# Performance work log

Measured on AMD Instinct MI355X. Metric: run time of the kernel, lower is better.

The kernel has to match this reference:

```python
import jax, jax.numpy as jnp
import numpy as np

N_NODES = 100000
N_EDGES = 3200000
C = 50           # out_channels (== in_channels here, so no zero-padding needed)
L = 3            # num_layers
EDGE_TYPES = 2


def setup_inputs() -> dict:
    key = jax.random.key(0)
    ks = jax.random.split(key, 12)
    s = 1.0 / np.sqrt(C)
    x = jax.random.normal(ks[0], (N_NODES, C), dtype=jnp.float32)
    edge_index = jax.random.randint(ks[1], (2, N_EDGES), 0, N_NODES)
    edge_attr = jax.random.randint(ks[2], (N_EDGES,), 0, EDGE_TYPES)
    conv_weight = jax.random.uniform(ks[3], (L, C, C), jnp.float32, -s, s)
    w_ih = jax.random.uniform(ks[4], (3 * C, C), jnp.float32, -s, s)
    w_hh = jax.random.uniform(ks[5], (3 * C, C), jnp.float32, -s, s)
    b_ih = jax.random.uniform(ks[6], (3 * C,), jnp.float32, -s, s)
    b_hh = jax.random.uniform(ks[7], (3 * C,), jnp.float32, -s, s)
    edge_emb = jax.random.normal(ks[8], (EDGE_TYPES, C), dtype=jnp.float32)
    lin_w = jax.random.uniform(ks[9], (C, C), jnp.float32, -s, s)
    lin_b = jax.random.uniform(ks[10], (C,), jnp.float32, -s, s)
    return dict(x=x, edge_index=edge_index, edge_attr=edge_attr,
                conv_weight=conv_weight, w_ih=w_ih, w_hh=w_hh,
                b_ih=b_ih, b_hh=b_hh, edge_emb=edge_emb,
                lin_w=lin_w, lin_b=lin_b)


def _gru_cell(m, h, w_ih, w_hh, b_ih, b_hh):
    # torch.nn.GRUCell math
    gi = m @ w_ih.T + b_ih            # [N, 3C]
    gh = h @ w_hh.T + b_hh            # [N, 3C]
    i_r, i_z, i_n = jnp.split(gi, 3, axis=-1)
    h_r, h_z, h_n = jnp.split(gh, 3, axis=-1)
    r = jax.nn.sigmoid(i_r + h_r)
    z = jax.nn.sigmoid(i_z + h_z)
    n = jnp.tanh(i_n + r * h_n)
    return (1.0 - z) * n + z * h


def reference(x, edge_index, edge_attr, conv_weight, w_ih, w_hh,
              b_ih, b_hh, edge_emb, lin_w, lin_b):
    # edge embeddings are computed but unused in the original forward
    _ = edge_emb[edge_attr]
    src, dst = edge_index[0], edge_index[1]  # flow: source -> target
    h = x  # in_channels == out_channels, so no padding
    for i in range(L):
        m = h @ conv_weight[i]                               # [N, C]
        msg = jnp.take(m, src, axis=0)                       # gather  [E, C]
        agg = jax.ops.segment_sum(msg, dst, num_segments=N_NODES)  # scatter-add
        h = _gru_cell(agg, h, w_ih, w_hh, b_ih, b_hh)
    out = jax.nn.relu(h) @ lin_w.T + lin_b
    return out
```

## Files before the change

### kernel.cpp

```cpp
#include <hip/hip_runtime.h>
#include <hip/hip_fp16.h>

#define N_NODES 100000
#define N_EDGES 3200000
#define C 50
#define PH 64
#define NH (N_NODES * PH)
#define NTILES (N_NODES / 16)
#define NB2 391
#define BSH2 8
#define BMSK2 255
#define BCAP2 9216
#define EPB 4096
#define EB  ((N_EDGES + EPB - 1) / EPB)
#define EPT (EPB / 256)

typedef _Float16 half8 __attribute__((ext_vector_type(8)));
typedef float floatx4 __attribute__((ext_vector_type(4)));


__global__ __launch_bounds__(256) void partition_kernel(const int* __restrict__ ei,
                                                        int* __restrict__ cnt,
                                                        unsigned int* __restrict__ pairs) {
    __shared__ int hist[NB2];
    __shared__ int base[NB2];
    int e0 = blockIdx.x * EPB;
    int b[EPT]; unsigned int p[EPT];
#pragma unroll
    for (int i = 0; i < EPT; ++i) {
        int e = e0 + i * 256 + threadIdx.x;
        bool ok = e < N_EDGES;
        int d = ok ? ei[N_EDGES + e] : 0;
        int s = ok ? ei[e] : 0;
        b[i] = ok ? (d >> BSH2) : -1;
        p[i] = ((unsigned)s << BSH2) | (unsigned)(d & BMSK2);
    }
    for (int t = threadIdx.x; t < NB2; t += 256) hist[t] = 0;
    __syncthreads();
#pragma unroll
    for (int i = 0; i < EPT; ++i)
        if (b[i] >= 0) atomicAdd(&hist[b[i]], 1);
    __syncthreads();
    for (int t = threadIdx.x; t < NB2; t += 256)
        base[t] = hist[t] ? (t * BCAP2 + atomicAdd(&cnt[t], hist[t])) : 0;
    __syncthreads();
    for (int t = threadIdx.x; t < NB2; t += 256) hist[t] = 0;
    __syncthreads();
#pragma unroll
    for (int i = 0; i < EPT; ++i) {
        if (b[i] >= 0) {
            int r = atomicAdd(&hist[b[i]], 1);
            pairs[base[b[i]] + r] = p[i];
        }
    }
}

__global__ __launch_bounds__(1024) void bscan_kernel(const int* __restrict__ cnt,
                                                     int* __restrict__ bucketOff) {
    __shared__ int buf[1024];
    int t = threadIdx.x;
    int v = (t < NB2) ? cnt[t] : 0;
    buf[t] = v;
    __syncthreads();
    for (int off = 1; off < 1024; off <<= 1) {
        int tv = (t >= off) ? buf[t - off] : 0;
        __syncthreads();
        buf[t] += tv;
        __syncthreads();
    }
    if (t < NB2) {
        int excl = buf[t] - v;
        bucketOff[t] = excl;
        if (t == NB2 - 1) bucketOff[NB2] = excl + v;
    }
}

__global__ __launch_bounds__(256) void bucket_fill_kernel(const unsigned int* __restrict__ pairs,
                                                          const int* __restrict__ cnt,
                                                          const int* __restrict__ bucketOff,
                                                          int* __restrict__ rowptr,
                                                          int* __restrict__ col) {
    __shared__ int deg[256];
    __shared__ int cur[256];
    int b = blockIdx.x;
    int nbase = b << BSH2;
    int n_e = cnt[b];
    int slot0 = b * BCAP2;
    int segB = bucketOff[b];
    int tid = threadIdx.x;
    deg[tid] = 0;
    __syncthreads();
    for (int e = tid; e < n_e; e += 256)
        atomicAdd(&deg[pairs[slot0 + e] & BMSK2], 1);
    __syncthreads();
    int v = deg[tid];
    cur[tid] = v;
    __syncthreads();
    for (int off = 1; off < 256; off <<= 1) {
        int t = (tid >= off) ? cur[tid - off] : 0;
        __syncthreads();
        cur[tid] += t;
        __syncthreads();
    }
    int excl = cur[tid] - v;
    int n = nbase + tid;
    if (n < N_NODES) rowptr[n] = segB + excl;
    __syncthreads();
    cur[tid] = excl;
    __syncthreads();
    for (int e = tid; e < n_e; e += 256) {
        unsigned int p = pairs[slot0 + e];
        int r = atomicAdd(&cur[p & BMSK2], 1);
        col[segB + r] = (int)(p >> BSH2);
    }
    if (b == 0 && tid == 0) rowptr[N_NODES] = N_EDGES;
}

__global__ __launch_bounds__(256) void init_kernel(const float* __restrict__ x,
                                                   const float* __restrict__ conv_w,
                                                   const float* __restrict__ w_ih,
                                                   const float* __restrict__ w_hh,
                                                   const float* __restrict__ lin_w,
                                                   _Float16* __restrict__ h0,
                                                   _Float16* __restrict__ wb,
                                                   int* __restrict__ cnt) {
    int t = blockIdx.x * 256 + threadIdx.x;
    if (t < NH) {
        int n = t >> 6, c = t & 63;
        h0[t] = (c < C) ? (_Float16)x[n * C + c] : (_Float16)0.f;
    }
    if (t < 10 * 4096) {
        int mat = t >> 12, idx = t & 4095, n = idx >> 6, k = idx & 63;
        float v = 0.f;
        if (n < C && k < C) {
            if (mat < 3)      v = conv_w[mat * C * C + k * C + n];
            else if (mat < 6) v = w_ih[((mat - 3) * C + n) * C + k];
            else if (mat < 9) v = w_hh[((mat - 6) * C + n) * C + k];
            else              v = lin_w[n * C + k];
        }
        wb[t] = (_Float16)v;
    }
    if (t < NB2) cnt[t] = 0;
}

__device__ inline half8 load_a16(const _Float16* __restrict__ base, int row, int ks, int lane) {
    return *(const half8*)(base + (size_t)row * PH + (ks << 5) + ((lane >> 4) << 3));
}

__device__ inline half8 load_b_frag(const _Float16* __restrict__ wb, int nt, int ks, int lane) {
    const _Float16* p = wb + (((nt << 4) + (lane & 15)) << 6) + (ks << 5) + ((lane >> 4) << 3);
    return *(const half8*)p;
}

__device__ inline half8 load_b_lds(const _Float16* swb, int mat, int nt, int ks, int lane) {
    return *(const half8*)(swb + mat * 4608 + ((nt << 4) + (lane & 15)) * 72 + (ks << 5) + ((lane >> 4) << 3));
}

__device__ inline float sigmoidf_(float x) { return 1.f / (1.f + __expf(-x)); }
__device__ inline float tanhf_(float x)    { return 2.f * sigmoidf_(2.f * x) - 1.f; }

__global__ __launch_bounds__(256) void gemm_conv(const _Float16* __restrict__ h,
                                                 const _Float16* __restrict__ wb,
                                                 _Float16* __restrict__ m_h) {
    int wid = threadIdx.x >> 6, lane = threadIdx.x & 63;
    int tile = blockIdx.x * 4 + wid;
    if (tile >= NTILES) return;
    int base = tile * 16;
    int arow = base + (lane & 15);
    half8 a0 = load_a16(h, arow, 0, lane);
    half8 a1 = load_a16(h, arow, 1, lane);
#pragma unroll
    for (int nt = 0; nt < 4; ++nt) {
        floatx4 acc = {0.f, 0.f, 0.f, 0.f};
        acc = __builtin_amdgcn_mfma_f32_16x16x32_f16(a0, load_b_frag(wb, nt, 0, lane), acc, 0, 0, 0);
        acc = __builtin_amdgcn_mfma_f32_16x16x32_f16(a1, load_b_frag(wb, nt, 1, lane), acc, 0, 0, 0);
        int col = (nt << 4) + (lane & 15);
#pragma unroll
        for (int e = 0; e < 4; ++e) {
            int row = base + ((lane >> 4) << 2) + e;
            m_h[(size_t)row * PH + col] = (_Float16)acc[e];
        }
    }
}

__global__ __launch_bounds__(256) void gemm_gru_conv(const _Float16* __restrict__ agg,
                                                     const _Float16* __restrict__ hin,
                                                     const _Float16* __restrict__ wb_ih,
                                                     const _Float16* __restrict__ wb_hh,
                                                     const float* __restrict__ b_ih,
                                                     const float* __restrict__ b_hh,
                                                     const _Float16* __restrict__ wb_conv,
                                                     _Float16* __restrict__ hout,
                                                     _Float16* __restrict__ m_h) {
    __shared__ __align__(16) _Float16 swb[6 * 4608];
    __shared__ __align__(16) _Float16 hlds[4][16][72];
    int wid = threadIdx.x >> 6, lane = threadIdx.x & 63;
    int tile = blockIdx.x * 4 + wid;
    bool act = tile < NTILES;
    int base = tile * 16;
    int lrow = lane & 15, lgrp = lane >> 4;
    for (int i = threadIdx.x; i < 3072; i += 256) {
        int g = i << 3;
        int m = g >> 12, rem = g & 4095, row = rem >> 6, colc = rem & 63;
        *(half8*)&swb[m * 4608 + row * 72 + colc] = *(const half8*)(wb_ih + g);
    }
    half8 aA[2], aH[2];
    if (act) {
        int arow = base + lrow;
#pragma unroll
        for (int ks = 0; ks < 2; ++ks) {
            aA[ks] = load_a16(agg, arow, ks, lane);
            aH[ks] = load_a16(hin, arow, ks, lane);
        }
        *(half8*)&hlds[wid][lrow][lgrp << 3]        = aH[0];
        *(half8*)&hlds[wid][lrow][32 + (lgrp << 3)] = aH[1];
    }
    __syncthreads();
    if (act) {
#pragma unroll
        for (int nt = 0; nt < 4; ++nt) {
            int colc = (nt << 4) + lrow;
            bool cok = colc < C;
            float r_[4], z_[4];
            {
                floatx4 aI = {0.f,0.f,0.f,0.f}, aHc = {0.f,0.f,0.f,0.f};
#pragma unroll
                for (int ks = 0; ks < 2; ++ks) {
                    aI  = __builtin_amdgcn_mfma_f32_16x16x32_f16(aA[ks], load_b_lds(swb, 0, nt, ks, lane), aI, 0, 0, 0);
                    aHc = __builtin_amdgcn_mfma_f32_16x16x32_f16(aH[ks], load_b_lds(swb, 3, nt, ks, lane), aHc, 0, 0, 0);
                }
                float bi = cok ? b_ih[colc] : 0.f;
                float bh = cok ? b_hh[colc] : 0.f;
#pragma unroll
                for (int e = 0; e < 4; ++e) r_[e] = sigmoidf_((aI[e] + bi) + (aHc[e] + bh));
            }
            {
                floatx4 aI = {0.f,0.f,0.f,0.f}, aHc = {0.f,0.f,0.f,0.f};
#pragma unroll
                for (int ks = 0; ks < 2; ++ks) {
                    aI  = __builtin_amdgcn_mfma_f32_16x16x32_f16(aA[ks], load_b_lds(swb, 1, nt, ks, lane), aI, 0, 0, 0);
                    aHc = __builtin_amdgcn_mfma_f32_16x16x32_f16(aH[ks], load_b_lds(swb, 4, nt, ks, lane), aHc, 0, 0, 0);
                }
                float bi = cok ? b_ih[C + colc] : 0.f;
                float bh = cok ? b_hh[C + colc] : 0.f;
#pragma unroll
                for (int e = 0; e < 4; ++e) z_[e] = sigmoidf_((aI[e] + bi) + (aHc[e] + bh));
            }
            {
                floatx4 aI = {0.f,0.f,0.f,0.f}, aHc = {0.f,0.f,0.f,0.f};
#pragma unroll
                for (int ks = 0; ks < 2; ++ks) {
                    aI  = __builtin_amdgcn_mfma_f32_16x16x32_f16(aA[ks], load_b_lds(swb, 2, nt, ks, lane), aI, 0, 0, 0);
                    aHc = __builtin_amdgcn_mfma_f32_16x16x32_f16(aH[ks], load_b_lds(swb, 5, nt, ks, lane), aHc, 0, 0, 0);
                }
                float bi = cok ? b_ih[2 * C + colc] : 0.f;
                float bh = cok ? b_hh[2 * C + colc] : 0.f;
#pragma unroll
                for (int e = 0; e < 4; ++e) {
                    int rl = (lgrp << 2) + e;
                    int row = base + rl;
                    _Float16 val = (_Float16)0.f;
                    if (cok) {
                        float hv = (float)hlds[wid][rl][colc];
                        float nn = tanhf_((aI[e] + bi) + r_[e] * (aHc[e] + bh));
                        float z = z_[e];
                        val = (_Float16)((1.f - z) * nn + z * hv);
                    }
                    hout[(size_t)row * PH + colc] = val;
                    hlds[wid][rl][colc] = val;
                }
            }
        }
    }
    __syncthreads();
    if (act) {
        half8 a0 = *(const half8*)&hlds[wid][lrow][lgrp << 3];
        half8 a1 = *(const half8*)&hlds[wid][lrow][32 + (lgrp << 3)];
#pragma unroll
        for (int nt = 0; nt < 4; ++nt) {
            floatx4 acc = {0.f, 0.f, 0.f, 0.f};
            acc = __builtin_amdgcn_mfma_f32_16x16x32_f16(a0, load_b_frag(wb_conv, nt, 0, lane), acc, 0, 0, 0);
            acc = __builtin_amdgcn_mfma_f32_16x16x32_f16(a1, load_b_frag(wb_conv, nt, 1, lane), acc, 0, 0, 0);
            int col = (nt << 4) + lrow;
#pragma unroll
            for (int e = 0; e < 4; ++e) {
                int row = base + (lgrp << 2) + e;
                m_h[(size_t)row * PH + col] = (_Float16)acc[e];
            }
        }
    }
}

__global__ __launch_bounds__(256) void gemm_gru_out(const _Float16* __restrict__ agg,
                                                    const _Float16* __restrict__ hin,
                                                    const _Float16* __restrict__ wb_ih,
                                                    const _Float16* __restrict__ wb_hh,
                                                    const float* __restrict__ b_ih,
                                                    const float* __restrict__ b_hh,
                                                    const _Float16* __restrict__ wb_out,
                                                    const float* __restrict__ lin_b,
                                                    float* __restrict__ out) {
    __shared__ __align__(16) _Float16 swb[6 * 4608];
    __shared__ __align__(16) _Float16 hlds[4][16][72];
    int wid = threadIdx.x >> 6, lane = threadIdx.x & 63;
    int tile = blockIdx.x * 4 + wid;
    bool act = tile < NTILES;
    int base = tile * 16;
    int lrow = lane & 15, lgrp = lane >> 4;
    for (int i = threadIdx.x; i < 3072; i += 256) {
        int g = i << 3;
        int m = g >> 12, rem = g & 4095, row = rem >> 6, colc = rem & 63;
        *(half8*)&swb[m * 4608 + row * 72 + colc] = *(const half8*)(wb_ih + g);
    }
    half8 aA[2], aH[2];
    if (act) {
        int arow = base + lrow;
#pragma unroll
        for (int ks = 0; ks < 2; ++ks) {
            aA[ks] = load_a16(agg, arow, ks, lane);
            aH[ks] = load_a16(hin, arow, ks, lane);
        }
        *(half8*)&hlds[wid][lrow][lgrp << 3]        = aH[0];
        *(half8*)&hlds[wid][lrow][32 + (lgrp << 3)] = aH[1];
    }
    __syncthreads();
    if (act) {
#pragma unroll
        for (int nt = 0; nt < 4; ++nt) {
            int colc = (nt << 4) + lrow;
            bool cok = colc < C;
            float r_[4], z_[4];
            {
                floatx4 aI = {0.f,0.f,0.f,0.f}, aHc = {0.f,0.f,0.f,0.f};
#pragma unroll
                for (int ks = 0; ks < 2; ++ks) {
                    aI  = __builtin_amdgcn_mfma_f32_16x16x32_f16(aA[ks], load_b_lds(swb, 0, nt, ks, lane), aI, 0, 0, 0);
                    aHc = __builtin_amdgcn_mfma_f32_16x16x32_f16(aH[ks], load_b_lds(swb, 3, nt, ks, lane), aHc, 0, 0, 0);
                }
                float bi = cok ? b_ih[colc] : 0.f;
                float bh = cok ? b_hh[colc] : 0.f;
#pragma unroll
                for (int e = 0; e < 4; ++e) r_[e] = sigmoidf_((aI[e] + bi) + (aHc[e] + bh));
            }
            {
                floatx4 aI = {0.f,0.f,0.f,0.f}, aHc = {0.f,0.f,0.f,0.f};
#pragma unroll
                for (int ks = 0; ks < 2; ++ks) {
                    aI  = __builtin_amdgcn_mfma_f32_16x16x32_f16(aA[ks], load_b_lds(swb, 1, nt, ks, lane), aI, 0, 0, 0);
                    aHc = __builtin_amdgcn_mfma_f32_16x16x32_f16(aH[ks], load_b_lds(swb, 4, nt, ks, lane), aHc, 0, 0, 0);
                }
                float bi = cok ? b_ih[C + colc] : 0.f;
                float bh = cok ? b_hh[C + colc] : 0.f;
#pragma unroll
                for (int e = 0; e < 4; ++e) z_[e] = sigmoidf_((aI[e] + bi) + (aHc[e] + bh));
            }
            {
                floatx4 aI = {0.f,0.f,0.f,0.f}, aHc = {0.f,0.f,0.f,0.f};
#pragma unroll
                for (int ks = 0; ks < 2; ++ks) {
                    aI  = __builtin_amdgcn_mfma_f32_16x16x32_f16(aA[ks], load_b_lds(swb, 2, nt, ks, lane), aI, 0, 0, 0);
                    aHc = __builtin_amdgcn_mfma_f32_16x16x32_f16(aH[ks], load_b_lds(swb, 5, nt, ks, lane), aHc, 0, 0, 0);
                }
                float bi = cok ? b_ih[2 * C + colc] : 0.f;
                float bh = cok ? b_hh[2 * C + colc] : 0.f;
#pragma unroll
                for (int e = 0; e < 4; ++e) {
                    int rl = (lgrp << 2) + e;
                    _Float16 val = (_Float16)0.f;
                    if (cok) {
                        float hv = (float)hlds[wid][rl][colc];
                        float nn = tanhf_((aI[e] + bi) + r_[e] * (aHc[e] + bh));
                        float z = z_[e];
                        float h3 = (1.f - z) * nn + z * hv;
                        val = (_Float16)(h3 > 0.f ? h3 : 0.f);
                    }
                    hlds[wid][rl][colc] = val;
                }
            }
        }
    }
    __syncthreads();
    if (act) {
        half8 a0 = *(const half8*)&hlds[wid][lrow][lgrp << 3];
        half8 a1 = *(const half8*)&hlds[wid][lrow][32 + (lgrp << 3)];
#pragma unroll
        for (int nt = 0; nt < 4; ++nt) {
            floatx4 acc = {0.f, 0.f, 0.f, 0.f};
            acc = __builtin_amdgcn_mfma_f32_16x16x32_f16(a0, load_b_frag(wb_out, nt, 0, lane), acc, 0, 0, 0);
            acc = __builtin_amdgcn_mfma_f32_16x16x32_f16(a1, load_b_frag(wb_out, nt, 1, lane), acc, 0, 0, 0);
            int col = (nt << 4) + lrow;
            if (col < C) {
                float b = lin_b[col];
#pragma unroll
                for (int e = 0; e < 4; ++e) {
                    int row = base + (lgrp << 2) + e;
                    out[(size_t)row * C + col] = acc[e] + b;
                }
            }
        }
    }
}

__global__ __launch_bounds__(256) void gather_kernel(const __half* __restrict__ m_h,
                                                     const int* __restrict__ rowptr,
                                                     const int* __restrict__ col,
                                                     _Float16* __restrict__ agg) {
    int w = (blockIdx.x * 256 + threadIdx.x) >> 6;
    int lane = threadIdx.x & 63;
    if (w >= N_NODES) return;
    int start = rowptr[w], end = rowptr[w + 1];
    int j = lane >> 3, q = lane & 7;
    bool qok = (q < 7);
    int hoff = qok ? (q * 8) : 48;
    float acc0 = 0.f, acc1 = 0.f, acc2 = 0.f, acc3 = 0.f;
    float acc4 = 0.f, acc5 = 0.f, acc6 = 0.f, acc7 = 0.f;

    for (int base = start; base < end; base += 64) {
        int cidx = base + lane;
        int cols = col[cidx < N_EDGES ? cidx : (N_EDGES - 1)];
        int cnt = end - base; if (cnt > 64) cnt = 64;
        int nt8 = (cnt + 7) >> 3;
#pragma unroll 4
        for (int t = 0; t < nt8; ++t) {
            int rel = 8 * t + j;
            int s = __shfl(cols, rel);
            bool valid = qok && (rel < cnt);
            const uint4 v = *reinterpret_cast<const uint4*>(m_h + (size_t)s * PH + hoff);
            float2 f0 = __half22float2(*reinterpret_cast<const __half2*>(&v.x));
            float2 f1 = __half22float2(*reinterpret_cast<const __half2*>(&v.y));
            float2 f2 = __half22float2(*reinterpret_cast<const __half2*>(&v.z));
            float2 f3 = __half22float2(*reinterpret_cast<const __half2*>(&v.w));
            acc0 += valid ? f0.x : 0.f;  acc1 += valid ? f0.y : 0.f;
            acc2 += valid ? f1.x : 0.f;  acc3 += valid ? f1.y : 0.f;
            acc4 += valid ? f2.x : 0.f;  acc5 += valid ? f2.y : 0.f;
            acc6 += valid ? f3.x : 0.f;  acc7 += valid ? f3.y : 0.f;
        }
    }
#pragma unroll
    for (int s = 8; s <= 32; s <<= 1) {
        acc0 += __shfl_xor(acc0, s); acc1 += __shfl_xor(acc1, s);
        acc2 += __shfl_xor(acc2, s); acc3 += __shfl_xor(acc3, s);
        acc4 += __shfl_xor(acc4, s); acc5 += __shfl_xor(acc5, s);
        acc6 += __shfl_xor(acc6, s); acc7 += __shfl_xor(acc7, s);
    }
    if (j == 0) {
        if (qok) {
            half8 o;
            o[0] = (_Float16)acc0; o[1] = (_Float16)acc1;
            o[2] = (_Float16)acc2; o[3] = (_Float16)acc3;
            o[4] = (_Float16)acc4; o[5] = (_Float16)acc5;
            o[6] = (_Float16)acc6; o[7] = (_Float16)acc7;
            *reinterpret_cast<half8*>(agg + (size_t)w * PH + q * 8) = o;
        } else {
            half8 z = {};
            *reinterpret_cast<half8*>(agg + (size_t)w * PH + 56) = z;
        }
    }
}

extern "C" void kernel_launch(void* const* d_in, const int* in_sizes, int n_in,
                              void* d_out, int out_size, void* d_ws, size_t ws_size,
                              hipStream_t stream) {
    const float* x      = (const float*)d_in[0];
    const int*   ei     = (const int*)  d_in[1];
    const float* conv_w = (const float*)d_in[3];
    const float* w_ih   = (const float*)d_in[4];
    const float* w_hh   = (const float*)d_in[5];
    const float* b_ih   = (const float*)d_in[6];
    const float* b_hh   = (const float*)d_in[7];
    const float* lin_w  = (const float*)d_in[9];
    const float* lin_b  = (const float*)d_in[10];
    float* out = (float*)d_out;

    _Float16* h0  = (_Float16*)d_ws;
    _Float16* h1  = h0 + NH;
    _Float16* agg = h1 + NH;
    _Float16* m_h = agg + NH;
    _Float16* wb  = m_h + NH;
    unsigned int* pairs = (unsigned int*)agg;
    int* col       = (int*)(wb + 10 * 4096);
    int* rowptr    = col + N_EDGES;
    int* cnt       = rowptr + N_NODES + 1;
    int* bucketOff = cnt + NB2;

    const int initBlocks = (NH + 255) / 256;
    const int waveBlocks = (N_NODES * 64 + 255) / 256;
    const int gemmBlocks = (NTILES + 3) / 4;

    init_kernel<<<initBlocks, 256, 0, stream>>>(x, conv_w, w_ih, w_hh, lin_w, h0, wb, cnt);

    partition_kernel<<<EB, 256, 0, stream>>>(ei, cnt, pairs);
    bscan_kernel<<<1, 1024, 0, stream>>>(cnt, bucketOff);
    bucket_fill_kernel<<<NB2, 256, 0, stream>>>(pairs, cnt, bucketOff, rowptr, col);

    gemm_conv<<<gemmBlocks, 256, 0, stream>>>(h0, wb + 0 * 4096, m_h);
    gather_kernel<<<waveBlocks, 256, 0, stream>>>((const __half*)m_h, rowptr, col, agg);
    gemm_gru_conv<<<gemmBlocks, 256, 0, stream>>>(agg, h0, wb + 3 * 4096, wb + 6 * 4096,
                                                  b_ih, b_hh, wb + 1 * 4096, h1, m_h);
    gather_kernel<<<waveBlocks, 256, 0, stream>>>((const __half*)m_h, rowptr, col, agg);
    gemm_gru_conv<<<gemmBlocks, 256, 0, stream>>>(agg, h1, wb + 3 * 4096, wb + 6 * 4096,
                                                  b_ih, b_hh, wb + 2 * 4096, h0, m_h);
    gather_kernel<<<waveBlocks, 256, 0, stream>>>((const __half*)m_h, rowptr, col, agg);
    gemm_gru_out<<<gemmBlocks, 256, 0, stream>>>(agg, h0, wb + 3 * 4096, wb + 6 * 4096,
                                                 b_ih, b_hh, wb + 9 * 4096, lin_b, out);
}
```

Measured before the change: 377.5 us.

## Fold conv weights into GRU input weights and gather raw hidden state

Because aggregation is linear, (A·h)·W_conv·W_ih^T equals A·h·(W_conv·W_ih^T). The per-layer product of conv weight and GRU input weight is now precomputed in init, so each layer gathers h directly and the separate conv GEMM and m_h write are gone. The GRU kernels stage combined ih and hh weights from separate buffers. It also halves edges per block in partitioning. The folded product is rounded to fp16, which slightly changes numerics, and init does more FMA work per weight element.

```diff
diff --git a/kernel.cpp b/kernel.cpp
--- a/kernel.cpp
+++ b/kernel.cpp
@@ -11,7 +11,7 @@
 #define BSH2 8
 #define BMSK2 255
 #define BCAP2 9216
-#define EPB 4096
+#define EPB 2048
 #define EB  ((N_EDGES + EPB - 1) / EPB)
 #define EPT (EPB / 256)
 
@@ -129,14 +129,23 @@
         int n = t >> 6, c = t & 63;
         h0[t] = (c < C) ? (_Float16)x[n * C + c] : (_Float16)0.f;
     }
-    if (t < 10 * 4096) {
+    if (t < 13 * 4096) {
         int mat = t >> 12, idx = t & 4095, n = idx >> 6, k = idx & 63;
         float v = 0.f;
         if (n < C && k < C) {
-            if (mat < 3)      v = conv_w[mat * C * C + k * C + n];
-            else if (mat < 6) v = w_ih[((mat - 3) * C + n) * C + k];
-            else if (mat < 9) v = w_hh[((mat - 6) * C + n) * C + k];
-            else              v = lin_w[n * C + k];
+            if (mat < 9) {
+                int l = mat / 3, g = mat - l * 3;
+                const float* wl = conv_w + l * C * C + k * C;
+                const float* wi = w_ih + (g * C + n) * C;
+                float acc = 0.f;
+#pragma unroll
+                for (int j = 0; j < C; ++j) acc = fmaf(wl[j], wi[j], acc);
+                v = acc;
+            } else if (mat < 12) {
+                v = w_hh[((mat - 9) * C + n) * C + k];
+            } else {
+                v = lin_w[n * C + k];
+            }
         }
         wb[t] = (_Float16)v;
     }
@@ -159,39 +168,22 @@
 __device__ inline float sigmoidf_(float x) { return 1.f / (1.f + __expf(-x)); }
 __device__ inline float tanhf_(float x)    { return 2.f * sigmoidf_(2.f * x) - 1.f; }
 
-__global__ __launch_bounds__(256) void gemm_conv(const _Float16* __restrict__ h,
-                                                 const _Float16* __restrict__ wb,
-                                                 _Float16* __restrict__ m_h) {
-    int wid = threadIdx.x >> 6, lane = threadIdx.x & 63;
-    int tile = blockIdx.x * 4 + wid;
-    if (tile >= NTILES) return;
-    int base = tile * 16;
-    int arow = base + (lane & 15);
-    half8 a0 = load_a16(h, arow, 0, lane);
-    half8 a1 = load_a16(h, arow, 1, lane);
-#pragma unroll
-    for (int nt = 0; nt < 4; ++nt) {
-        floatx4 acc = {0.f, 0.f, 0.f, 0.f};
-        acc = __builtin_amdgcn_mfma_f32_16x16x32_f16(a0, load_b_frag(wb, nt, 0, lane), acc, 0, 0, 0);
-        acc = __builtin_amdgcn_mfma_f32_16x16x32_f16(a1, load_b_frag(wb, nt, 1, lane), acc, 0, 0, 0);
-        int col = (nt << 4) + (lane & 15);
-#pragma unroll
-        for (int e = 0; e < 4; ++e) {
-            int row = base + ((lane >> 4) << 2) + e;
-            m_h[(size_t)row * PH + col] = (_Float16)acc[e];
-        }
-    }
-}
-
-__global__ __launch_bounds__(256) void gemm_gru_conv(const _Float16* __restrict__ agg,
-                                                     const _Float16* __restrict__ hin,
-                                                     const _Float16* __restrict__ wb_ih,
-                                                     const _Float16* __restrict__ wb_hh,
-                                                     const float* __restrict__ b_ih,
-                                                     const float* __restrict__ b_hh,
-                                                     const _Float16* __restrict__ wb_conv,
-                                                     _Float16* __restrict__ hout,
-                                                     _Float16* __restrict__ m_h) {
+__device__ inline void stage_swb(_Float16* swb, const _Float16* ihp, const _Float16* hhp) {
+    for (int i = threadIdx.x; i < 3072; i += 256) {
+        int g = i << 3;
+        int m = g >> 12, rem = g & 4095, row = rem >> 6, colc = rem & 63;
+        const _Float16* src = (m < 3) ? (ihp + g) : (hhp + (g - 3 * 4096));
+        *(half8*)&swb[m * 4608 + row * 72 + colc] = *(const half8*)src;
+    }
+}
+
+__global__ __launch_bounds__(256) void gemm_gru(const _Float16* __restrict__ agg,
+                                                const _Float16* __restrict__ hin,
+                                                const _Float16* __restrict__ wb_ihc,
+                                                const _Float16* __restrict__ wb_hh,
+                                                const float* __restrict__ b_ih,
+                                                const float* __restrict__ b_hh,
+                                                _Float16* __restrict__ hout) {
     __shared__ __align__(16) _Float16 swb[6 * 4608];
     __shared__ __align__(16) _Float16 hlds[4][16][72];
     int wid = threadIdx.x >> 6, lane = threadIdx.x & 63;
@@ -199,11 +191,7 @@
     bool act = tile < NTILES;
     int base = tile * 16;
     int lrow = lane & 15, lgrp = lane >> 4;
-    for (int i = threadIdx.x; i < 3072; i += 256) {
-        int g = i << 3;
-        int m = g >> 12, rem = g & 4095, row = rem >> 6, colc = rem & 63;
-        *(half8*)&swb[m * 4608 + row * 72 + colc] = *(const half8*)(wb_ih + g);
-    }
+    stage_swb(swb, wb_ihc, wb_hh);
     half8 aA[2], aH[2];
     if (act) {
         int arow = base + lrow;
@@ -216,76 +204,57 @@
         *(half8*)&hlds[wid][lrow][32 + (lgrp << 3)] = aH[1];
     }
     __syncthreads();
-    if (act) {
-#pragma unroll
-        for (int nt = 0; nt < 4; ++nt) {
-            int colc = (nt << 4) + lrow;
-            bool cok = colc < C;
-            float r_[4], z_[4];
-            {
-                floatx4 aI = {0.f,0.f,0.f,0.f}, aHc = {0.f,0.f,0.f,0.f};
-#pragma unroll
-                for (int ks = 0; ks < 2; ++ks) {
-                    aI  = __builtin_amdgcn_mfma_f32_16x16x32_f16(aA[ks], load_b_lds(swb, 0, nt, ks, lane), aI, 0, 0, 0);
-                    aHc = __builtin_amdgcn_mfma_f32_16x16x32_f16(aH[ks], load_b_lds(swb, 3, nt, ks, lane), aHc, 0, 0, 0);
-                }
-                float bi = cok ? b_ih[colc] : 0.f;
-                float bh = cok ? b_hh[colc] : 0.f;
-#pragma unroll
-                for (int e = 0; e < 4; ++e) r_[e] = sigmoidf_((aI[e] + bi) + (aHc[e] + bh));
-            }
-            {
-                floatx4 aI = {0.f,0.f,0.f,0.f}, aHc = {0.f,0.f,0.f,0.f};
-#pragma unroll
-                for (int ks = 0; ks < 2; ++ks) {
-                    aI  = __builtin_amdgcn_mfma_f32_16x16x32_f16(aA[ks], load_b_lds(swb, 1, nt, ks, lane), aI, 0, 0, 0);
-                    aHc = __builtin_amdgcn_mfma_f32_16x16x32_f16(aH[ks], load_b_lds(swb, 4, nt, ks, lane), aHc, 0, 0, 0);
-                }
-                float bi = cok ? b_ih[C + colc] : 0.f;
-                float bh = cok ? b_hh[C + colc] : 0.f;
-#pragma unroll
-                for (int e = 0; e < 4; ++e) z_[e] = sigmoidf_((aI[e] + bi) + (aHc[e] + bh));
-            }
-            {
-                floatx4 aI = {0.f,0.f,0.f,0.f}, aHc = {0.f,0.f,0.f,0.f};
-#pragma unroll
-                for (int ks = 0; ks < 2; ++ks) {
-                    aI  = __builtin_amdgcn_mfma_f32_16x16x32_f16(aA[ks], load_b_lds(swb, 2, nt, ks, lane), aI, 0, 0, 0);
-                    aHc = __builtin_amdgcn_mfma_f32_16x16x32_f16(aH[ks], load_b_lds(swb, 5, nt, ks, lane), aHc, 0, 0, 0);
-                }
-                float bi = cok ? b_ih[2 * C + colc] : 0.f;
-                float bh = cok ? b_hh[2 * C + colc] : 0.f;
-#pragma unroll
-                for (int e = 0; e < 4; ++e) {
-                    int rl = (lgrp << 2) + e;
-                    int row = base + rl;
-                    _Float16 val = (_Float16)0.f;
-                    if (cok) {
-                        float hv = (float)hlds[wid][rl][colc];
-                        float nn = tanhf_((aI[e] + bi) + r_[e] * (aHc[e] + bh));
-                        float z = z_[e];
-                        val = (_Float16)((1.f - z) * nn + z * hv);
-                    }
-                    hout[(size_t)row * PH + colc] = val;
-                    hlds[wid][rl][colc] = val;
-                }
-            }
-        }
-    }
-    __syncthreads();
-    if (act) {
-        half8 a0 = *(const half8*)&hlds[wid][lrow][lgrp << 3];
-        half8 a1 = *(const half8*)&hlds[wid][lrow][32 + (lgrp << 3)];
-#pragma unroll
-        for (int nt = 0; nt < 4; ++nt) {
-            floatx4 acc = {0.f, 0.f, 0.f, 0.f};
-            acc = __builtin_amdgcn_mfma_f32_16x16x32_f16(a0, load_b_frag(wb_conv, nt, 0, lane), acc, 0, 0, 0);
-            acc = __builtin_amdgcn_mfma_f32_16x16x32_f16(a1, load_b_frag(wb_conv, nt, 1, lane), acc, 0, 0, 0);
-            int col = (nt << 4) + lrow;
+    if (!act) return;
+#pragma unroll
+    for (int nt = 0; nt < 4; ++nt) {
+        int colc = (nt << 4) + lrow;
+        bool cok = colc < C;
+        float r_[4], z_[4];
+        {
+            floatx4 aI = {0.f,0.f,0.f,0.f}, aHc = {0.f,0.f,0.f,0.f};
+#pragma unroll
+            for (int ks = 0; ks < 2; ++ks) {
+                aI  = __builtin_amdgcn_mfma_f32_16x16x32_f16(aA[ks], load_b_lds(swb, 0, nt, ks, lane), aI, 0, 0, 0);
+                aHc = __builtin_amdgcn_mfma_f32_16x16x32_f16(aH[ks], load_b_lds(swb, 3, nt, ks, lane), aHc, 0, 0, 0);
+            }
+            float bi = cok ? b_ih[colc] : 0.f;
+            float bh = cok ? b_hh[colc] : 0.f;
+#pragma unroll
+            for (int e = 0; e < 4; ++e) r_[e] = sigmoidf_((aI[e] + bi) + (aHc[e] + bh));
+        }
+        {
+            floatx4 aI = {0.f,0.f,0.f,0.f}, aHc = {0.f,0.f,0.f,0.f};
+#pragma unroll
+            for (int ks = 0; ks < 2; ++ks) {
+                aI  = __builtin_amdgcn_mfma_f32_16x16x32_f16(aA[ks], load_b_lds(swb, 1, nt, ks, lane), aI, 0, 0, 0);
+                aHc = __builtin_amdgcn_mfma_f32_16x16x32_f16(aH[ks], load_b_lds(swb, 4, nt, ks, lane), aHc, 0, 0, 0);
+            }
+            float bi = cok ? b_ih[C + colc] : 0.f;
+            float bh = cok ? b_hh[C + colc] : 0.f;
+#pragma unroll
+            for (int e = 0; e < 4; ++e) z_[e] = sigmoidf_((aI[e] + bi) + (aHc[e] + bh));
+        }
+        {
+            floatx4 aI = {0.f,0.f,0.f,0.f}, aHc = {0.f,0.f,0.f,0.f};
+#pragma unroll
+            for (int ks = 0; ks < 2; ++ks) {
+                aI  = __builtin_amdgcn_mfma_f32_16x16x32_f16(aA[ks], load_b_lds(swb, 2, nt, ks, lane), aI, 0, 0, 0);
+                aHc = __builtin_amdgcn_mfma_f32_16x16x32_f16(aH[ks], load_b_lds(swb, 5, nt, ks, lane), aHc, 0, 0, 0);
+            }
+            float bi = cok ? b_ih[2 * C + colc] : 0.f;
+            float bh = cok ? b_hh[2 * C + colc] : 0.f;
 #pragma unroll
             for (int e = 0; e < 4; ++e) {
-                int row = base + (lgrp << 2) + e;
-                m_h[(size_t)row * PH + col] = (_Float16)acc[e];
+                int rl = (lgrp << 2) + e;
+                int row = base + rl;
+                _Float16 val = (_Float16)0.f;
+                if (cok) {
+                    float hv = (float)hlds[wid][rl][colc];
+                    float nn = tanhf_((aI[e] + bi) + r_[e] * (aHc[e] + bh));
+                    float z = z_[e];
+                    val = (_Float16)((1.f - z) * nn + z * hv);
+                }
+                hout[(size_t)row * PH + colc] = val;
             }
         }
     }
@@ -293,7 +262,7 @@
 
 __global__ __launch_bounds__(256) void gemm_gru_out(const _Float16* __restrict__ agg,
                                                     const _Float16* __restrict__ hin,
-                                                    const _Float16* __restrict__ wb_ih,
+                                                    const _Float16* __restrict__ wb_ihc,
                                                     const _Float16* __restrict__ wb_hh,
                                                     const float* __restrict__ b_ih,
                                                     const float* __restrict__ b_hh,
@@ -307,11 +276,7 @@
     bool act = tile < NTILES;
     int base = tile * 16;
     int lrow = lane & 15, lgrp = lane >> 4;
-    for (int i = threadIdx.x; i < 3072; i += 256) {
-        int g = i << 3;
-        int m = g >> 12, rem = g & 4095, row = rem >> 6, colc = rem & 63;
-        *(half8*)&swb[m * 4608 + row * 72 + colc] = *(const half8*)(wb_ih + g);
-    }
+    stage_swb(swb, wb_ihc, wb_hh);
     half8 aA[2], aH[2];
     if (act) {
         int arow = base + lrow;
@@ -401,7 +366,7 @@
     }
 }
 
-__global__ __launch_bounds__(256) void gather_kernel(const __half* __restrict__ m_h,
+__global__ __launch_bounds__(256) void gather_kernel(const __half* __restrict__ h,
                                                      const int* __restrict__ rowptr,
                                                      const int* __restrict__ col,
                                                      _Float16* __restrict__ agg) {
@@ -425,7 +390,7 @@
             int rel = 8 * t + j;
             int s = __shfl(cols, rel);
             bool valid = qok && (rel < cnt);
-            const uint4 v = *reinterpret_cast<const uint4*>(m_h + (size_t)s * PH + hoff);
+            const uint4 v = *reinterpret_cast<const uint4*>(h + (size_t)s * PH + hoff);
             float2 f0 = __half22float2(*reinterpret_cast<const __half2*>(&v.x));
             float2 f1 = __half22float2(*reinterpret_cast<const __half2*>(&v.y));
             float2 f2 = __half22float2(*reinterpret_cast<const __half2*>(&v.z));
@@ -475,10 +440,10 @@
     _Float16* h0  = (_Float16*)d_ws;
     _Float16* h1  = h0 + NH;
     _Float16* agg = h1 + NH;
-    _Float16* m_h = agg + NH;
-    _Float16* wb  = m_h + NH;
+    _Float16* scratch = agg + NH;
+    _Float16* wb  = scratch + NH;
     unsigned int* pairs = (unsigned int*)agg;
-    int* col       = (int*)(wb + 10 * 4096);
+    int* col       = (int*)(wb + 13 * 4096);
     int* rowptr    = col + N_EDGES;
     int* cnt       = rowptr + N_NODES + 1;
     int* bucketOff = cnt + NB2;
@@ -493,14 +458,13 @@
     bscan_kernel<<<1, 1024, 0, stream>>>(cnt, bucketOff);
     bucket_fill_kernel<<<NB2, 256, 0, stream>>>(pairs, cnt, bucketOff, rowptr, col);
 
-    gemm_conv<<<gemmBlocks, 256, 0, stream>>>(h0, wb + 0 * 4096, m_h);
-    gather_kernel<<<waveBlocks, 256, 0, stream>>>((const __half*)m_h, rowptr, col, agg);
-    gemm_gru_conv<<<gemmBlocks, 256, 0, stream>>>(agg, h0, wb + 3 * 4096, wb + 6 * 4096,
-                                                  b_ih, b_hh, wb + 1 * 4096, h1, m_h);
-    gather_kernel<<<waveBlocks, 256, 0, stream>>>((const __half*)m_h, rowptr, col, agg);
-    gemm_gru_conv<<<gemmBlocks, 256, 0, stream>>>(agg, h1, wb + 3 * 4096, wb + 6 * 4096,
-                                                  b_ih, b_hh, wb + 2 * 4096, h0, m_h);
-    gather_kernel<<<waveBlocks, 256, 0, stream>>>((const __half*)m_h, rowptr, col, agg);
-    gemm_gru_out<<<gemmBlocks, 256, 0, stream>>>(agg, h0, wb + 3 * 4096, wb + 6 * 4096,
-                                                 b_ih, b_hh, wb + 9 * 4096, lin_b, out);
-}
+    gather_kernel<<<waveBlocks, 256, 0, stream>>>((const __half*)h0, rowptr, col, agg);
+    gemm_gru<<<gemmBlocks, 256, 0, stream>>>(agg, h0, wb + 0 * 3 * 4096, wb + 9 * 4096,
+                                             b_ih, b_hh, h1);
+    gather_kernel<<<waveBlocks, 256, 0, stream>>>((const __half*)h1, rowptr, col, agg);
+    gemm_gru<<<gemmBlocks, 256, 0, stream>>>(agg, h1, wb + 1 * 3 * 4096, wb + 9 * 4096,
+                                             b_ih, b_hh, h0);
+    gather_kernel<<<waveBlocks, 256, 0, stream>>>((const __half*)h0, rowptr, col, agg);
+    gemm_gru_out<<<gemmBlocks, 256, 0, stream>>>(agg, h0, wb + 2 * 3 * 4096, wb + 9 * 4096,
+                                                 b_ih, b_hh, wb + 12 * 4096, lin_b, out);
+}
```

New measurement: 390.8 us. 1.04x slower.
